# Performance work log

Hardware: AMD Instinct MI355X
Metric: run time of the kernel (lower is better)

The kernel has to match this reference:

```python
import jax, jax.numpy as jnp
import numpy as np
import math

D = 256   # d_model / hidden_size
Q = 256   # q_num (query-side nodes)
K = 512   # k_num (key-side nodes)
NEG = -9e15


def _forward(q_enc, k_enc, rel_k, rel_v, k_adj,
             W_glob, b_glob, W_gv0, b_gv0, W_gv1, b_gv1,
             W_gq, b_gq, W_lq, b_lq,
             W_locgate, b_locgate, W_gate, b_gate):
    d = q_enc.shape[-1]
    scale = 1.0 / math.sqrt(d)
    act = jnp.tanh  # activation_func='tanh'

    # --- global sigmoid blending of k_enc with the mean query encoding ---
    q_glob_enc = jnp.mean(q_enc, axis=0)                       # [d]
    k_s = jax.nn.sigmoid((q_glob_enc @ W_glob + b_glob) @ k_enc.T * scale)  # [K]
    k_s = k_s[:, None]                                         # [K,1]
    g_1 = q_glob_enc @ W_gv0 + b_gv0                           # [d]
    k_1 = k_enc @ W_gv1 + b_gv1                                # [K,d]
    k_enc2 = (1.0 - k_s) * k_1 + k_s * g_1                     # [K,d]

    # --- global relation-aware attention over k nodes ---
    q_glob = q_enc @ W_gq + b_gq                               # [Q,d]
    qk_logit = q_glob @ k_enc2.T                               # [Q,K]
    qk_r = jnp.einsum('qd,qkd->qk', q_glob, rel_k)             # [Q,K]
    glob_attn = jax.nn.softmax(act((qk_logit + qk_r) * scale), axis=-1)  # [Q,K]

    # --- local adjacency-masked attention ---
    q_loc = q_enc @ W_lq + b_lq                                # [Q,d]
    qnk_logit = q_loc @ k_enc2.T                               # [Q,K]
    qnk_r = jnp.einsum('qd,qkd->qk', q_loc, rel_k)             # [Q,K]
    loc_attn = act((qnk_logit + qnk_r) * scale)                # [Q,K]
    # loc_weight_rep[q,i,j] = loc_attn[q,j]  (repeat + view in torch)
    mask = (k_adj != 0)[None, :, :]                            # [1,K,K]
    masked = jnp.where(mask, loc_attn[:, None, :], NEG)        # [Q,K,K]
    attn_adj_norm = jax.nn.softmax(masked, axis=-1)            # [Q,K,K]
    k_loc = jnp.einsum('qij,jd->qid', attn_adj_norm, k_enc2)   # [Q,K,d]

    # --- local gate between neighborhood value and self value ---
    # sigmoid(cat([k_loc, k_self]) @ W_locgate + b); k_self is broadcast k_enc2
    Wg1, Wg2 = W_locgate[:d], W_locgate[d:]                    # [d,1] each
    gate_logit = (jnp.einsum('qid,d->qi', k_loc, Wg1[:, 0])
                  + (k_enc2 @ Wg2)[None, :, 0] + b_locgate[0])  # [Q,K]
    loc_gate = jax.nn.sigmoid(gate_logit)[..., None]           # [Q,K,1]
    k_awr = loc_gate * k_loc + (1.0 - loc_gate) * k_enc2[None, :, :]  # [Q,K,d]

    # --- aggregate with global attention + relation values ---
    k_matmul = jnp.einsum('qk,qkd->qd', glob_attn, k_awr)      # [Q,d]
    k_r_matmul = jnp.einsum('qk,qkd->qd', glob_attn, rel_v)    # [Q,d]
    q_enc_new = k_matmul + k_r_matmul                          # [Q,d]

    # --- residual gate ---
    Wq1, Wq2 = W_gate[:d], W_gate[d:]
    gate = jax.nn.sigmoid(q_enc_new @ Wq1 + q_enc @ Wq2 + b_gate)  # [Q,1]
    h = gate * q_enc_new + (1.0 - gate) * q_enc                # [Q,d]
    return h


def setup_inputs() -> dict:
    key = jax.random.key(0)
    ks = jax.random.split(key, 16)
    def w(k, shape):
        return jax.random.normal(k, shape, jnp.float32) * 0.02
    return {
        'q_enc': jax.random.normal(ks[0], (Q, D), jnp.float32),
        'k_enc': jax.random.normal(ks[1], (K, D), jnp.float32),
        'rel_k': jax.random.normal(ks[2], (Q, K, D), jnp.float32) * 0.1,
        'rel_v': jax.random.normal(ks[3], (Q, K, D), jnp.float32) * 0.1,
        'k_adj': jax.random.randint(ks[4], (K, K), 0, 2, jnp.int64) if jax.config.jax_enable_x64 else jax.random.randint(ks[4], (K, K), 0, 2, jnp.int32),
        'W_glob': w(ks[5], (D, D)), 'b_glob': jnp.zeros((D,), jnp.float32),
        'W_gv0': w(ks[6], (D, D)), 'b_gv0': jnp.zeros((D,), jnp.float32),
        'W_gv1': w(ks[7], (D, D)), 'b_gv1': jnp.zeros((D,), jnp.float32),
        'W_gq': w(ks[8], (D, D)), 'b_gq': jnp.zeros((D,), jnp.float32),
        'W_lq': w(ks[9], (D, D)), 'b_lq': jnp.zeros((D,), jnp.float32),
        'W_locgate': w(ks[10], (2 * D, 1)), 'b_locgate': jnp.zeros((1,), jnp.float32),
        'W_gate': w(ks[11], (2 * D, 1)), 'b_gate': jnp.zeros((1,), jnp.float32),
    }


def reference(q_enc, k_enc, rel_k, rel_v, k_adj,
              W_glob, b_glob, W_gv0, b_gv0, W_gv1, b_gv1,
              W_gq, b_gq, W_lq, b_lq,
              W_locgate, b_locgate, W_gate, b_gate):
    return _forward(q_enc, k_enc, rel_k, rel_v, k_adj,
                    W_glob, b_glob, W_gv0, b_gv0, W_gv1, b_gv1,
                    W_gq, b_gq, W_lq, b_lq,
                    W_locgate, b_locgate, W_gate, b_gate)
```

## Files before the change

### kernel.cpp

```cpp
#include <hip/hip_runtime.h>
#include <math.h>

#define QN 256
#define KN 512
#define DN 256
#define SCALE 0.0625f

typedef __attribute__((ext_vector_type(8))) short short8v;
typedef __attribute__((ext_vector_type(4))) float f32x4;

__device__ __forceinline__ float sigf(float x){ return 1.0f/(1.0f+expf(-x)); }

__device__ __forceinline__ unsigned short f2bf(float x){
  unsigned u = __float_as_uint(x);
  unsigned r = (u + 0x7FFFu + ((u >> 16) & 1u)) >> 16;
  return (unsigned short)r;
}

__device__ __forceinline__ short8v ld8(const unsigned short* p){
  ushort4 a = *(const ushort4*)p;
  ushort4 b = *(const ushort4*)(p + 16);
  short8v r;
  r[0]=(short)a.x; r[1]=(short)a.y; r[2]=(short)a.z; r[3]=(short)a.w;
  r[4]=(short)b.x; r[5]=(short)b.y; r[6]=(short)b.z; r[7]=(short)b.w;
  return r;
}

__device__ __forceinline__ float wave_red(float v){
  #pragma unroll
  for (int off = 32; off; off >>= 1) v += __shfl_down(v, off);
  return v;
}

__global__ void kA2(const float* __restrict__ q_enc,
                    const float* __restrict__ W_glob, const float* __restrict__ W_gv0,
                    float* __restrict__ party0, float* __restrict__ party1,
                    const int* __restrict__ kadj, unsigned short* __restrict__ mbf){
  __shared__ float sm[256][9];
  __shared__ float qm[8];
  int b = blockIdx.x, t = threadIdx.x;
  int j0 = b*8;
  #pragma unroll
  for (int i = 0; i < 8; ++i){
    int gi = b*2048 + i*256 + t;
    int4 v = ((const int4*)kadj)[gi];
    ushort4 o;
    o.x = v.x ? 0x3F80 : 0; o.y = v.y ? 0x3F80 : 0;
    o.z = v.z ? 0x3F80 : 0; o.w = v.w ? 0x3F80 : 0;
    ((ushort4*)mbf)[gi] = o;
  }
  float4 lo = *(const float4*)(q_enc + (size_t)t*DN + j0);
  float4 hi = *(const float4*)(q_enc + (size_t)t*DN + j0 + 4);
  sm[t][0]=lo.x; sm[t][1]=lo.y; sm[t][2]=lo.z; sm[t][3]=lo.w;
  sm[t][4]=hi.x; sm[t][5]=hi.y; sm[t][6]=hi.z; sm[t][7]=hi.w;
  __syncthreads();
  #pragma unroll
  for (int s = 128; s > 0; s >>= 1){
    if (t < s){
      #pragma unroll
      for (int j = 0; j < 8; ++j) sm[t][j] += sm[t+s][j];
    }
    __syncthreads();
  }
  if (t < 8) qm[t] = sm[0][t] * (1.0f/QN);
  __syncthreads();
  float a0 = 0.f, a1 = 0.f;
  #pragma unroll
  for (int j = 0; j < 8; ++j){
    float s = qm[j];
    a0 = fmaf(s, W_glob[(size_t)(j0+j)*DN + t], a0);
    a1 = fmaf(s, W_gv0[(size_t)(j0+j)*DN + t], a1);
  }
  party0[b*256 + t] = a0; party1[b*256 + t] = a1;
}

__global__ void k23(const float* __restrict__ k_enc,
                    const float* __restrict__ W_gv1, const float* __restrict__ b_gv1,
                    const float* __restrict__ party0, const float* __restrict__ party1,
                    const float* __restrict__ b_glob, const float* __restrict__ b_gv0,
                    const float* __restrict__ W_locgate,
                    float* __restrict__ k_enc2, float* __restrict__ cvec,
                    float* __restrict__ gl2,
                    const float* __restrict__ q_enc,
                    const float* __restrict__ W_gq, const float* __restrict__ b_gq,
                    const float* __restrict__ W_lq, const float* __restrict__ b_lq,
                    float* __restrict__ q_glob, float* __restrict__ q_loc){
  __shared__ float sh1[256];
  __shared__ float red8[8];
  int bid = blockIdx.x, t = threadIdx.x;
  int w = t >> 6, lane = t & 63;
  if (bid < 512){
    int k = bid;
    float tg = b_glob[t], g1v = b_gv0[t];
    #pragma unroll 8
    for (int b2 = 0; b2 < 32; ++b2){
      tg  += party0[b2*256 + t];
      g1v += party1[b2*256 + t];
    }
    float kv = k_enc[(size_t)k*DN + t];
    sh1[t] = kv;
    float part = wave_red(kv * tg);
    if (lane == 0) red8[w] = part;
    __syncthreads();
    float dot = red8[0] + red8[1] + red8[2] + red8[3];
    float ks = sigf(dot * SCALE);
    float acc = b_gv1[t];
    #pragma unroll 8
    for (int j = 0; j < DN; ++j) acc = fmaf(sh1[j], W_gv1[(size_t)j*DN + t], acc);
    float v = (1.f - ks)*acc + ks*g1v;
    k_enc2[(size_t)k*DN + t] = v;
    float pc = wave_red(v * W_locgate[t]);
    float pg = wave_red(v * W_locgate[DN + t]);
    __syncthreads();
    if (lane == 0){ red8[w] = pc; red8[4 + w] = pg; }
    __syncthreads();
    if (t == 0) cvec[k] = red8[0] + red8[1] + red8[2] + red8[3];
    if (t == 1) gl2[k]  = red8[4] + red8[5] + red8[6] + red8[7];
  } else {
    int q = bid - 512;
    sh1[t] = q_enc[(size_t)q*DN + t];
    __syncthreads();
    float a = b_gq[t], b = b_lq[t];
    #pragma unroll 8
    for (int j = 0; j < DN; ++j){
      float s = sh1[j];
      a = fmaf(s, W_gq[(size_t)j*DN + t], a);
      b = fmaf(s, W_lq[(size_t)j*DN + t], b);
    }
    q_glob[(size_t)q*DN + t] = a; q_loc[(size_t)q*DN + t] = b;
  }
}

__global__ void kb2(const float* __restrict__ rel_k,
                    const float* __restrict__ q_glob, const float* __restrict__ q_loc,
                    const float* __restrict__ ke2, const float* __restrict__ cvec,
                    float* __restrict__ exs, float* __restrict__ ev,
                    unsigned short* __restrict__ ebf, unsigned short* __restrict__ ecbf){
  int t = threadIdx.x;
  int wv = t >> 6, lane = t & 63;
  int g = lane >> 4, l16 = lane & 15;
  int b = blockIdx.x;
  int q = b >> 5;
  int k = (b & 31)*16 + wv*4 + g;
  float p1 = 0.f, p2 = 0.f, p3 = 0.f, p4 = 0.f;
  #pragma unroll
  for (int it = 0; it < 4; ++it){
    int d = it*64 + l16*4;
    f32x4 x  = __builtin_nontemporal_load((const f32x4*)(rel_k + ((size_t)q*KN + k)*DN + d));
    float4 a  = *(const float4*)(q_glob + (size_t)q*DN + d);
    float4 bb = *(const float4*)(q_loc  + (size_t)q*DN + d);
    float4 c  = *(const float4*)(ke2    + (size_t)k*DN + d);
    p1 += x[0]*a.x + x[1]*a.y + x[2]*a.z + x[3]*a.w;
    p2 += x[0]*bb.x + x[1]*bb.y + x[2]*bb.z + x[3]*bb.w;
    p3 += c.x*a.x + c.y*a.y + c.z*a.z + c.w*a.w;
    p4 += c.x*bb.x + c.y*bb.y + c.z*bb.z + c.w*bb.w;
  }
  #pragma unroll
  for (int off = 8; off; off >>= 1){
    p1 += __shfl_down(p1, off); p2 += __shfl_down(p2, off);
    p3 += __shfl_down(p3, off); p4 += __shfl_down(p4, off);
  }
  if (l16 == 0){
    size_t idx = (size_t)q*KN + k;
    exs[idx] = expf(tanhf((p1 + p3)*SCALE));
    float evv = expf(tanhf((p2 + p4)*SCALE));
    ev[idx] = evv;
    ebf[idx] = f2bf(evv);
    ecbf[idx] = f2bf(evv * cvec[k]);
  }
}

__global__ __launch_bounds__(256) void kcA2m(const unsigned short* __restrict__ ebf,
                                             const unsigned short* __restrict__ ecbf,
                                             const unsigned short* __restrict__ mbf,
                                             const float* __restrict__ exs,
                                             const float* __restrict__ gl2,
                                             const float* __restrict__ blg_p,
                                             unsigned short* __restrict__ wvbf,
                                             float* __restrict__ v2){
  __shared__ unsigned short Ae[16*520];
  __shared__ unsigned short Ac[16*520];
  __shared__ unsigned short Bm[64*520];
  int t = threadIdx.x;
  int i0 = blockIdx.x*64, q0 = blockIdx.y*16;
  #pragma unroll
  for (int it = 0; it < 4; ++it){
    int c = t + 256*it; int row = c >> 6, col = (c & 63)*8;
    *(uint4*)&Ae[row*520 + col] = *(const uint4*)&ebf[(size_t)(q0+row)*KN + col];
    *(uint4*)&Ac[row*520 + col] = *(const uint4*)&ecbf[(size_t)(q0+row)*KN + col];
  }
  #pragma unroll
  for (int it = 0; it < 16; ++it){
    int c = t + 256*it; int row = c >> 6, col = (c & 63)*8;
    *(uint4*)&Bm[row*520 + col] = *(const uint4*)&mbf[(size_t)(i0+row)*KN + col];
  }
  __syncthreads();
  int w = t >> 6, l = t & 63;
  int g16 = l >> 4, l16 = l & 15;
  f32x4 aS = {0.f,0.f,0.f,0.f}, aN = {0.f,0.f,0.f,0.f};
  const unsigned short* pe = &Ae[l16*520];
  const unsigned short* pc = &Ac[l16*520];
  const unsigned short* pb = &Bm[(16*w + l16)*520];
  #pragma unroll
  for (int kk = 0; kk < 16; ++kk){
    int k0 = kk*32 + 4*g16;
    short8v fa = ld8(pe + k0);
    short8v fc = ld8(pc + k0);
    short8v fb = ld8(pb + k0);
    aS = __builtin_amdgcn_mfma_f32_16x16x32_bf16(fa, fb, aS, 0, 0, 0);
    aN = __builtin_amdgcn_mfma_f32_16x16x32_bf16(fc, fb, aN, 0, 0, 0);
  }
  float blg = blg_p[0];
  int i = i0 + 16*w + l16;
  float gli = gl2[i];
  #pragma unroll
  for (int r = 0; r < 4; ++r){
    int q = q0 + 4*g16 + r;
    size_t idx = (size_t)q*KN + i;
    float s = aS[r], n = aN[r];
    float lgv = sigf(n/s + gli + blg);
    float ex = exs[idx];
    wvbf[idx] = f2bf(ex*lgv/s);
    v2[idx] = ex*(1.f - lgv);
  }
}

__global__ __launch_bounds__(256) void kcC2m(const unsigned short* __restrict__ wvbf,
                                             const unsigned short* __restrict__ mbf,
                                             const float* __restrict__ ev,
                                             const float* __restrict__ v2,
                                             float* __restrict__ coef){
  __shared__ unsigned short Aw[16*520];
  __shared__ unsigned short Bm2[512*72];
  int t = threadIdx.x;
  int j0 = blockIdx.x*64, q0 = blockIdx.y*16;
  #pragma unroll
  for (int it = 0; it < 4; ++it){
    int c = t + 256*it; int row = c >> 6, col = (c & 63)*8;
    *(uint4*)&Aw[row*520 + col] = *(const uint4*)&wvbf[(size_t)(q0+row)*KN + col];
  }
  #pragma unroll
  for (int it = 0; it < 16; ++it){
    int c = t + 256*it; int row = c >> 3, col = (c & 7)*8;
    *(uint4*)&Bm2[row*72 + col] = *(const uint4*)&mbf[(size_t)row*KN + j0 + col];
  }
  __syncthreads();
  int w = t >> 6, l = t & 63;
  int g16 = l >> 4, l16 = l & 15;
  f32x4 aU = {0.f,0.f,0.f,0.f};
  const unsigned short* pa = &Aw[l16*520];
  int nn = 16*w + l16;
  #pragma unroll
  for (int kk = 0; kk < 16; ++kk){
    int k0 = kk*32 + 4*g16;
    short8v fa = ld8(pa + k0);
    short8v fb;
    #pragma unroll
    for (int e = 0; e < 4; ++e){
      fb[e]   = (short)Bm2[(k0+e)*72 + nn];
      fb[4+e] = (short)Bm2[(k0+16+e)*72 + nn];
    }
    aU = __builtin_amdgcn_mfma_f32_16x16x32_bf16(fa, fb, aU, 0, 0, 0);
  }
  int j = j0 + nn;
  #pragma unroll
  for (int r = 0; r < 4; ++r){
    int q = q0 + 4*g16 + r;
    size_t idx = (size_t)q*KN + j;
    coef[idx] = aU[r]*ev[idx] + v2[idx];
  }
}

__global__ __launch_bounds__(1024) void kDE(const float* __restrict__ relv,
                                            const float* __restrict__ ke2,
                                            const float* __restrict__ exs,
                                            const float* __restrict__ coef,
                                            const float* __restrict__ q_enc,
                                            const float* __restrict__ W_gate,
                                            const float* __restrict__ b_gate,
                                            float* __restrict__ out){
  __shared__ float red[512];
  __shared__ float4 pacc[16][64];
  int q = blockIdx.x, t = threadIdx.x, w = t >> 6, lane = t & 63;
  if (t < 512) red[t] = exs[(size_t)q*KN + t];
  __syncthreads();
  #pragma unroll
  for (int s = 256; s > 0; s >>= 1){
    if (t < s) red[t] += red[t+s];
    __syncthreads();
  }
  float invs = 1.0f / red[0];
  float4 acc = make_float4(0.f,0.f,0.f,0.f);
  int kbase = w*32;
  #pragma unroll 8
  for (int kk = 0; kk < 32; ++kk){
    int k = kbase + kk;
    float gk = exs[(size_t)q*KN + k];
    float ck = coef[(size_t)q*KN + k];
    f32x4 xv = __builtin_nontemporal_load((const f32x4*)(relv + ((size_t)q*KN + k)*DN) + lane);
    float4 kv = ((const float4*)(ke2 + (size_t)k*DN))[lane];
    acc.x = fmaf(gk, xv[0], fmaf(ck, kv.x, acc.x));
    acc.y = fmaf(gk, xv[1], fmaf(ck, kv.y, acc.y));
    acc.z = fmaf(gk, xv[2], fmaf(ck, kv.z, acc.z));
    acc.w = fmaf(gk, xv[3], fmaf(ck, kv.w, acc.w));
  }
  pacc[w][lane] = acc;
  __syncthreads();
  if (t < 64){
    float4 r = pacc[0][t];
    #pragma unroll
    for (int w2 = 1; w2 < 16; ++w2){
      float4 p = pacc[w2][t];
      r.x += p.x; r.y += p.y; r.z += p.z; r.w += p.w;
    }
    r.x *= invs; r.y *= invs; r.z *= invs; r.w *= invs;
    float4 qe = ((const float4*)(q_enc + (size_t)q*DN))[t];
    float4 w1 = ((const float4*)(W_gate))[t];
    float4 w2v = ((const float4*)(W_gate + DN))[t];
    float pd = r.x*w1.x + r.y*w1.y + r.z*w1.z + r.w*w1.w
             + qe.x*w2v.x + qe.y*w2v.y + qe.z*w2v.z + qe.w*w2v.w;
    #pragma unroll
    for (int off = 32; off; off >>= 1) pd += __shfl_down(pd, off);
    float gate = sigf(__shfl(pd, 0) + b_gate[0]);
    float4 h;
    h.x = gate*r.x + (1.f-gate)*qe.x;
    h.y = gate*r.y + (1.f-gate)*qe.y;
    h.z = gate*r.z + (1.f-gate)*qe.z;
    h.w = gate*r.w + (1.f-gate)*qe.w;
    ((float4*)(out + (size_t)q*DN))[t] = h;
  }
}

extern "C" void kernel_launch(void* const* d_in, const int* in_sizes, int n_in,
                              void* d_out, int out_size, void* d_ws, size_t ws_size,
                              hipStream_t stream){
  const float* q_enc     = (const float*)d_in[0];
  const float* k_enc     = (const float*)d_in[1];
  const float* rel_k     = (const float*)d_in[2];
  const float* rel_v     = (const float*)d_in[3];
  const int*   k_adj     = (const int*)  d_in[4];
  const float* W_glob    = (const float*)d_in[5];
  const float* b_glob    = (const float*)d_in[6];
  const float* W_gv0     = (const float*)d_in[7];
  const float* b_gv0     = (const float*)d_in[8];
  const float* W_gv1     = (const float*)d_in[9];
  const float* b_gv1     = (const float*)d_in[10];
  const float* W_gq      = (const float*)d_in[11];
  const float* b_gq      = (const float*)d_in[12];
  const float* W_lq      = (const float*)d_in[13];
  const float* b_lq      = (const float*)d_in[14];
  const float* W_locgate = (const float*)d_in[15];
  const float* b_locgate = (const float*)d_in[16];
  const float* W_gate    = (const float*)d_in[17];
  const float* b_gate    = (const float*)d_in[18];
  float* out = (float*)d_out;

  float* ws = (float*)d_ws;
  float* party0   = ws;
  float* party1   = party0 + 8192;
  float* k_enc2   = party1 + 8192;
  float* cvec     = k_enc2 + 131072;
  float* gl2      = cvec + 512;
  float* q_glob   = gl2 + 512;
  float* q_loc    = q_glob + 65536;
  float* exs      = q_loc + 65536;
  float* evb      = exs + 131072;
  float* v2       = evb + 131072;
  float* coef     = v2 + 131072;
  unsigned short* mbf  = (unsigned short*)(coef + 131072);
  unsigned short* ebf  = mbf + 262144;
  unsigned short* ecbf = ebf + 131072;
  unsigned short* wvbf = ecbf + 131072;

  kA2<<<32, 256, 0, stream>>>(q_enc, W_glob, W_gv0, party0, party1, k_adj, mbf);
  k23<<<768, 256, 0, stream>>>(k_enc, W_gv1, b_gv1, party0, party1, b_glob, b_gv0,
                               W_locgate, k_enc2, cvec, gl2,
                               q_enc, W_gq, b_gq, W_lq, b_lq, q_glob, q_loc);
  kb2<<<8192, 256, 0, stream>>>(rel_k, q_glob, q_loc, k_enc2, cvec,
                                exs, evb, ebf, ecbf);
  kcA2m<<<dim3(8, 16), 256, 0, stream>>>(ebf, ecbf, mbf, exs, gl2, b_locgate, wvbf, v2);
  kcC2m<<<dim3(8, 16), 256, 0, stream>>>(wvbf, mbf, evb, v2, coef);
  kDE<<<256, 1024, 0, stream>>>(rel_v, k_enc2, exs, coef, q_enc, W_gate, b_gate, out);
}
```

Measured before the change: 89.87 us.

## Fuse rel_v weighted reduction into rel_k scoring kernel with per-slice partials

The rel_v streaming (exs-weighted sum over k) moves out of the final kernel and into the rel_k scoring kernel. Each block now covers a 64-key slice for one query, reads rel_k and rel_v rows together, and writes per-slice partial sums to a new workspace buffer. The final kernel then only adds the coef·k_enc2 term on top of those partials. Both large tensors are streamed in one pass by more blocks, and the heavy load moves off the tail kernel. The cost is extra partial-buffer traffic, higher register pressure from holding rel_v vectors, and a grid reduced from 8192 to 2048 blocks.

After: 90.07 us. Within noise of the previous version (+0.2%).

```diff
diff --git a/kernel.cpp b/kernel.cpp
--- a/kernel.cpp
+++ b/kernel.cpp
@@ -131,42 +131,88 @@
   }
 }
 
-__global__ void kb2(const float* __restrict__ rel_k,
+__global__ __launch_bounds__(256) void kbf(const float* __restrict__ rel_k,
+                    const float* __restrict__ rel_v,
                     const float* __restrict__ q_glob, const float* __restrict__ q_loc,
                     const float* __restrict__ ke2, const float* __restrict__ cvec,
                     float* __restrict__ exs, float* __restrict__ ev,
-                    unsigned short* __restrict__ ebf, unsigned short* __restrict__ ecbf){
+                    unsigned short* __restrict__ ebf, unsigned short* __restrict__ ecbf,
+                    float* __restrict__ part){
+  __shared__ f32x4 sacc[4][16][4];
   int t = threadIdx.x;
   int wv = t >> 6, lane = t & 63;
   int g = lane >> 4, l16 = lane & 15;
   int b = blockIdx.x;
-  int q = b >> 5;
-  int k = (b & 31)*16 + wv*4 + g;
-  float p1 = 0.f, p2 = 0.f, p3 = 0.f, p4 = 0.f;
-  #pragma unroll
-  for (int it = 0; it < 4; ++it){
-    int d = it*64 + l16*4;
-    f32x4 x  = __builtin_nontemporal_load((const f32x4*)(rel_k + ((size_t)q*KN + k)*DN + d));
-    float4 a  = *(const float4*)(q_glob + (size_t)q*DN + d);
-    float4 bb = *(const float4*)(q_loc  + (size_t)q*DN + d);
-    float4 c  = *(const float4*)(ke2    + (size_t)k*DN + d);
-    p1 += x[0]*a.x + x[1]*a.y + x[2]*a.z + x[3]*a.w;
-    p2 += x[0]*bb.x + x[1]*bb.y + x[2]*bb.z + x[3]*bb.w;
-    p3 += c.x*a.x + c.y*a.y + c.z*a.z + c.w*a.w;
-    p4 += c.x*bb.x + c.y*bb.y + c.z*bb.z + c.w*bb.w;
-  }
-  #pragma unroll
-  for (int off = 8; off; off >>= 1){
-    p1 += __shfl_down(p1, off); p2 += __shfl_down(p2, off);
-    p3 += __shfl_down(p3, off); p4 += __shfl_down(p4, off);
-  }
-  if (l16 == 0){
-    size_t idx = (size_t)q*KN + k;
-    exs[idx] = expf(tanhf((p1 + p3)*SCALE));
-    float evv = expf(tanhf((p2 + p4)*SCALE));
-    ev[idx] = evv;
-    ebf[idx] = f2bf(evv);
-    ecbf[idx] = f2bf(evv * cvec[k]);
+  int q = b >> 3, slice = b & 7;
+  int base = lane & 48;
+  f32x4 racc[4];
+  #pragma unroll
+  for (int it = 0; it < 4; ++it) racc[it] = (f32x4){0.f,0.f,0.f,0.f};
+  #pragma unroll 1
+  for (int kq = 0; kq < 4; ++kq){
+    int k = slice*64 + kq*16 + wv*4 + g;
+    size_t rowoff = ((size_t)q*KN + k)*DN;
+    float p1 = 0.f, p2 = 0.f, p3 = 0.f, p4 = 0.f;
+    f32x4 y[4];
+    #pragma unroll
+    for (int it = 0; it < 4; ++it){
+      int d = it*64 + l16*4;
+      f32x4 x = __builtin_nontemporal_load((const f32x4*)(rel_k + rowoff + d));
+      y[it]   = __builtin_nontemporal_load((const f32x4*)(rel_v + rowoff + d));
+      float4 a  = *(const float4*)(q_glob + (size_t)q*DN + d);
+      float4 bb = *(const float4*)(q_loc  + (size_t)q*DN + d);
+      float4 c  = *(const float4*)(ke2    + (size_t)k*DN + d);
+      p1 += x[0]*a.x + x[1]*a.y + x[2]*a.z + x[3]*a.w;
+      p2 += x[0]*bb.x + x[1]*bb.y + x[2]*bb.z + x[3]*bb.w;
+      p3 += c.x*a.x + c.y*a.y + c.z*a.z + c.w*a.w;
+      p4 += c.x*bb.x + c.y*bb.y + c.z*bb.z + c.w*bb.w;
+    }
+    #pragma unroll
+    for (int off = 8; off; off >>= 1){
+      p1 += __shfl_down(p1, off); p2 += __shfl_down(p2, off);
+      p3 += __shfl_down(p3, off); p4 += __shfl_down(p4, off);
+    }
+    float p13 = __shfl(p1 + p3, base);
+    float p24 = __shfl(p2 + p4, base);
+    float exv = expf(tanhf(p13*SCALE));
+    float evv = expf(tanhf(p24*SCALE));
+    if (l16 == 0){
+      size_t idx = (size_t)q*KN + k;
+      exs[idx] = exv;
+      ev[idx] = evv;
+      ebf[idx] = f2bf(evv);
+      ecbf[idx] = f2bf(evv * cvec[k]);
+    }
+    #pragma unroll
+    for (int it = 0; it < 4; ++it){
+      racc[it][0] = fmaf(exv, y[it][0], racc[it][0]);
+      racc[it][1] = fmaf(exv, y[it][1], racc[it][1]);
+      racc[it][2] = fmaf(exv, y[it][2], racc[it][2]);
+      racc[it][3] = fmaf(exv, y[it][3], racc[it][3]);
+    }
+  }
+  #pragma unroll
+  for (int h = 16; h <= 32; h <<= 1){
+    #pragma unroll
+    for (int it = 0; it < 4; ++it){
+      racc[it][0] += __shfl_xor(racc[it][0], h);
+      racc[it][1] += __shfl_xor(racc[it][1], h);
+      racc[it][2] += __shfl_xor(racc[it][2], h);
+      racc[it][3] += __shfl_xor(racc[it][3], h);
+    }
+  }
+  if (lane < 16){
+    #pragma unroll
+    for (int it = 0; it < 4; ++it) sacc[wv][lane][it] = racc[it];
+  }
+  __syncthreads();
+  if (t < 64){
+    int it = t >> 4, lb = t & 15;
+    f32x4 r0 = sacc[0][lb][it], r1 = sacc[1][lb][it];
+    f32x4 r2 = sacc[2][lb][it], r3 = sacc[3][lb][it];
+    f32x4 r = r0 + r1 + r2 + r3;
+    int d = it*64 + lb*4;
+    *(f32x4*)(part + ((size_t)slice*QN + q)*DN + d) = r;
   }
 }
 
@@ -271,18 +317,18 @@
   }
 }
 
-__global__ __launch_bounds__(1024) void kDE(const float* __restrict__ relv,
-                                            const float* __restrict__ ke2,
-                                            const float* __restrict__ exs,
-                                            const float* __restrict__ coef,
-                                            const float* __restrict__ q_enc,
-                                            const float* __restrict__ W_gate,
-                                            const float* __restrict__ b_gate,
-                                            float* __restrict__ out){
+__global__ __launch_bounds__(512) void kE2(const float* __restrict__ ke2,
+                                           const float* __restrict__ exs,
+                                           const float* __restrict__ coef,
+                                           const float* __restrict__ part,
+                                           const float* __restrict__ q_enc,
+                                           const float* __restrict__ W_gate,
+                                           const float* __restrict__ b_gate,
+                                           float* __restrict__ out){
   __shared__ float red[512];
-  __shared__ float4 pacc[16][64];
+  __shared__ float4 pacc[8][64];
   int q = blockIdx.x, t = threadIdx.x, w = t >> 6, lane = t & 63;
-  if (t < 512) red[t] = exs[(size_t)q*KN + t];
+  red[t] = exs[(size_t)q*KN + t];
   __syncthreads();
   #pragma unroll
   for (int s = 256; s > 0; s >>= 1){
@@ -290,26 +336,25 @@
     __syncthreads();
   }
   float invs = 1.0f / red[0];
-  float4 acc = make_float4(0.f,0.f,0.f,0.f);
-  int kbase = w*32;
+  f32x4 pv = *(const f32x4*)(part + ((size_t)w*QN + q)*DN + lane*4);
+  float4 acc = make_float4(pv[0], pv[1], pv[2], pv[3]);
+  int kbase = w*64;
   #pragma unroll 8
-  for (int kk = 0; kk < 32; ++kk){
+  for (int kk = 0; kk < 64; ++kk){
     int k = kbase + kk;
-    float gk = exs[(size_t)q*KN + k];
     float ck = coef[(size_t)q*KN + k];
-    f32x4 xv = __builtin_nontemporal_load((const f32x4*)(relv + ((size_t)q*KN + k)*DN) + lane);
     float4 kv = ((const float4*)(ke2 + (size_t)k*DN))[lane];
-    acc.x = fmaf(gk, xv[0], fmaf(ck, kv.x, acc.x));
-    acc.y = fmaf(gk, xv[1], fmaf(ck, kv.y, acc.y));
-    acc.z = fmaf(gk, xv[2], fmaf(ck, kv.z, acc.z));
-    acc.w = fmaf(gk, xv[3], fmaf(ck, kv.w, acc.w));
+    acc.x = fmaf(ck, kv.x, acc.x);
+    acc.y = fmaf(ck, kv.y, acc.y);
+    acc.z = fmaf(ck, kv.z, acc.z);
+    acc.w = fmaf(ck, kv.w, acc.w);
   }
   pacc[w][lane] = acc;
   __syncthreads();
   if (t < 64){
     float4 r = pacc[0][t];
     #pragma unroll
-    for (int w2 = 1; w2 < 16; ++w2){
+    for (int w2 = 1; w2 < 8; ++w2){
       float4 p = pacc[w2][t];
       r.x += p.x; r.y += p.y; r.z += p.z; r.w += p.w;
     }
@@ -367,7 +412,8 @@
   float* evb      = exs + 131072;
   float* v2       = evb + 131072;
   float* coef     = v2 + 131072;
-  unsigned short* mbf  = (unsigned short*)(coef + 131072);
+  float* part     = coef + 131072;
+  unsigned short* mbf  = (unsigned short*)(part + 524288);
   unsigned short* ebf  = mbf + 262144;
   unsigned short* ecbf = ebf + 131072;
   unsigned short* wvbf = ecbf + 131072;
@@ -376,9 +422,9 @@
   k23<<<768, 256, 0, stream>>>(k_enc, W_gv1, b_gv1, party0, party1, b_glob, b_gv0,
                                W_locgate, k_enc2, cvec, gl2,
                                q_enc, W_gq, b_gq, W_lq, b_lq, q_glob, q_loc);
-  kb2<<<8192, 256, 0, stream>>>(rel_k, q_glob, q_loc, k_enc2, cvec,
-                                exs, evb, ebf, ecbf);
+  kbf<<<2048, 256, 0, stream>>>(rel_k, rel_v, q_glob, q_loc, k_enc2, cvec,
+                                exs, evb, ebf, ecbf, part);
   kcA2m<<<dim3(8, 16), 256, 0, stream>>>(ebf, ecbf, mbf, exs, gl2, b_locgate, wvbf, v2);
   kcC2m<<<dim3(8, 16), 256, 0, stream>>>(wvbf, mbf, evb, v2, coef);
-  kDE<<<256, 1024, 0, stream>>>(rel_v, k_enc2, exs, coef, q_enc, W_gate, b_gate, out);
-}
+  kE2<<<256, 512, 0, stream>>>(k_enc2, exs, coef, part, q_enc, W_gate, b_gate, out);
+}
```
